# Kernel optimization log

Measured on AMD Instinct MI355X. Metric: run time of the kernel, lower is better.

Reference implementation:

```python
import jax, jax.numpy as jnp
import numpy as np

N, E, D_IN, HEADS, C = 100000, 1600000, 128, 4, 32  # C = out_channels per head


def setup_inputs() -> dict:
    key = jax.random.key(0)
    ks = jax.random.split(key, 10)
    s = 1.0 / np.sqrt(D_IN)
    return {
        "x": jax.random.normal(ks[0], (N, D_IN), jnp.float32),
        "edge_index": jax.random.randint(ks[1], (2, E), 0, N, jnp.int64),
        "Wq": jax.random.normal(ks[2], (D_IN, HEADS * C), jnp.float32) * s,
        "bq": jnp.zeros((HEADS * C,), jnp.float32),
        "Wk": jax.random.normal(ks[3], (D_IN, HEADS * C), jnp.float32) * s,
        "bk": jnp.zeros((HEADS * C,), jnp.float32),
        "Wv": jax.random.normal(ks[4], (D_IN, HEADS * C), jnp.float32) * s,
        "bv": jnp.zeros((HEADS * C,), jnp.float32),
        "Wskip": jax.random.normal(ks[5], (D_IN, HEADS * C), jnp.float32) * s,
        "bskip": jnp.zeros((HEADS * C,), jnp.float32),
    }


def reference(x, edge_index, Wq, bq, Wk, bk, Wv, bv, Wskip, bskip):
    n = x.shape[0]
    src, dst = edge_index[0], edge_index[1]  # message flows src (j) -> dst (i)
    q = (x @ Wq + bq).reshape(n, HEADS, C)
    k = (x @ Wk + bk).reshape(n, HEADS, C)
    v = (x @ Wv + bv).reshape(n, HEADS, C)

    # per-edge attention logits [E, H]
    alpha = jnp.einsum('ehc,ehc->eh', q[dst], k[src]) / jnp.sqrt(jnp.float32(C))

    # segment softmax over incoming edges of each target node
    m = jax.ops.segment_max(alpha, dst, num_segments=n)          # [N, H]
    p = jnp.exp(alpha - m[dst])                                   # [E, H]
    z = jax.ops.segment_sum(p, dst, num_segments=n)               # [N, H]
    w = p / (z[dst] + 1e-16)                                      # [E, H]

    # softmax-weighted scatter aggregation of values
    out = jax.ops.segment_sum(v[src] * w[:, :, None], dst, num_segments=n)
    out = out.reshape(n, HEADS * C)

    # root/skip connection (beta=False default: plain add)
    out = out + x @ Wskip + bskip
    return out
```

## Files before the change

### kernel.cpp

```cpp
#include <hip/hip_runtime.h>

#define DIN 128
#define NHEADS 4
#define CH 32
#define MT 128
#define CHUNK 4096
#define NPB 256
#define EPB_IT 25

typedef _Float16 h8 __attribute__((ext_vector_type(8)));
typedef float f4 __attribute__((ext_vector_type(4)));

__global__ __launch_bounds__(256) void cvt_x(
    const float* __restrict__ x, _Float16* __restrict__ xh, int n4)
{
    int i = blockIdx.x * 256 + threadIdx.x;
    if (i >= n4) return;
    float4 xv = reinterpret_cast<const float4*>(x)[i];
    _Float16 h[4] = {(_Float16)xv.x, (_Float16)xv.y, (_Float16)xv.z, (_Float16)xv.w};
    reinterpret_cast<uint2*>(xh)[i] = *reinterpret_cast<uint2*>(h);
}

__global__ __launch_bounds__(256) void prep_w(
    const float* __restrict__ Wq, const float* __restrict__ Wk,
    const float* __restrict__ Wv, const float* __restrict__ Wsk,
    _Float16* __restrict__ wt)
{
    int i = blockIdx.x * 256 + threadIdx.x;
    if (i >= 4 * 16384) return;
    int mat = i >> 14;
    int rem = i & 16383;
    int n  = rem >> 7;
    int kk = rem & 127;
    const float* W = (mat == 0) ? Wq : (mat == 1) ? Wk : (mat == 2) ? Wv : Wsk;
    wt[i] = (_Float16)W[kk * 128 + n];
}

__global__ __launch_bounds__(256) void qkvs_mfma(
    const _Float16* __restrict__ xh, const _Float16* __restrict__ wt,
    const float* __restrict__ bq, const float* __restrict__ bk,
    const float* __restrict__ bv, const float* __restrict__ bsk,
    _Float16* __restrict__ qh, _Float16* __restrict__ kvh,
    float* __restrict__ outskip, int N)
{
    __shared__ _Float16 As[MT * 128];
    const int t = threadIdx.x;
    const int rowBase = blockIdx.x * MT;
    const int mat = blockIdx.y;

    for (int i = t; i < MT * 16; i += 256) {
        int r  = i >> 4;
        int c8 = i & 15;
        uint4 val = make_uint4(0u, 0u, 0u, 0u);
        int gr = rowBase + r;
        if (gr < N)
            val = reinterpret_cast<const uint4*>(xh)[(size_t)gr * 16 + c8];
        *reinterpret_cast<uint4*>(&As[r * 128 + ((c8 ^ (r & 7)) << 3)]) = val;
    }
    __syncthreads();

    const int wid  = t >> 6;
    const int l    = t & 63;
    const int lm   = l & 15;
    const int quad = l >> 4;

    const _Float16* __restrict__ Bsrc = wt + (size_t)mat * 16384;

    f4 acc[2][8];
    #pragma unroll
    for (int ms = 0; ms < 2; ++ms)
        #pragma unroll
        for (int nt = 0; nt < 8; ++nt)
            acc[ms][nt] = (f4){0.f, 0.f, 0.f, 0.f};

    #pragma unroll
    for (int kq = 0; kq < 4; ++kq) {
        const int c8 = kq * 4 + quad;
        const int k0 = c8 << 3;
        h8 a0 = *reinterpret_cast<const h8*>(
            &As[(wid * 32 + lm) * 128 + ((c8 ^ (lm & 7)) << 3)]);
        h8 a1 = *reinterpret_cast<const h8*>(
            &As[(wid * 32 + 16 + lm) * 128 + ((c8 ^ (lm & 7)) << 3)]);
        #pragma unroll
        for (int nt = 0; nt < 8; ++nt) {
            h8 b = *reinterpret_cast<const h8*>(
                &Bsrc[(size_t)(nt * 16 + lm) * 128 + k0]);
            acc[0][nt] = __builtin_amdgcn_mfma_f32_16x16x32_f16(a0, b, acc[0][nt], 0, 0, 0);
            acc[1][nt] = __builtin_amdgcn_mfma_f32_16x16x32_f16(a1, b, acc[1][nt], 0, 0, 0);
        }
    }

    const float* bias = (mat == 0) ? bq : (mat == 1) ? bk : (mat == 2) ? bv : bsk;

    #pragma unroll
    for (int ms = 0; ms < 2; ++ms) {
        #pragma unroll
        for (int nt = 0; nt < 8; ++nt) {
            int col = nt * 16 + lm;
            float bsv = bias[col];
            #pragma unroll
            for (int i2 = 0; i2 < 4; ++i2) {
                int row = rowBase + wid * 32 + ms * 16 + quad * 4 + i2;
                if (row < N) {
                    float val = acc[ms][nt][i2] + bsv;
                    if (mat == 3)
                        outskip[(size_t)row * 128 + col] = val;
                    else if (mat == 0)
                        qh[(size_t)row * 128 + col] = (_Float16)val;
                    else {
                        size_t off = (size_t)row * 256 + ((col >> 2) << 3)
                                   + (col & 3) + ((mat == 2) ? 4 : 0);
                        kvh[off] = (_Float16)val;
                    }
                }
            }
        }
    }
}

__global__ __launch_bounds__(256) void bucket_hist(
    const int* __restrict__ ei, int* __restrict__ bcnt, int E, int nb)
{
    __shared__ int lds[512];
    for (int b = threadIdx.x; b < nb; b += 256) lds[b] = 0;
    __syncthreads();
    for (long long i = (long long)blockIdx.x * 256 + threadIdx.x; i < E;
         i += (long long)gridDim.x * 256)
        atomicAdd(&lds[ei[(size_t)E + i] >> 8], 1);
    __syncthreads();
    for (int b = threadIdx.x; b < nb; b += 256)
        if (lds[b]) atomicAdd(&bcnt[b], lds[b]);
}

__global__ __launch_bounds__(512) void scan_buckets(
    const int* __restrict__ bcnt, int* __restrict__ boff,
    int* __restrict__ bcur, int nb)
{
    __shared__ int ws[8];
    int t = threadIdx.x, lane = t & 63, wid = t >> 6;
    int v = (t < nb) ? bcnt[t] : 0;
    int s = v;
    #pragma unroll
    for (int off = 1; off < 64; off <<= 1) {
        int n = __shfl_up(s, off);
        if (lane >= off) s += n;
    }
    if (lane == 63) ws[wid] = s;
    __syncthreads();
    int add = 0;
    for (int w = 0; w < wid; ++w) add += ws[w];
    int excl = s - v + add;
    if (t < nb) { boff[t] = excl; bcur[t] = excl; }
    if (t == nb - 1) boff[nb] = excl + v;
}

__global__ __launch_bounds__(256) void bucket_scatter(
    const int* __restrict__ ei, int* __restrict__ bcur,
    uint2* __restrict__ pairs, int E, int nb)
{
    __shared__ int cnt[512];
    int t = threadIdx.x;
    for (int b = t; b < nb; b += 256) cnt[b] = 0;
    __syncthreads();

    long long e0 = (long long)blockIdx.x * (256 * EPB_IT);
    int ps[EPB_IT], pd[EPB_IT];
    #pragma unroll
    for (int j = 0; j < EPB_IT; ++j) {
        long long e = e0 + j * 256 + t;
        if (e < E) {
            ps[j] = ei[e];
            pd[j] = ei[(size_t)E + e];
            atomicAdd(&cnt[pd[j] >> 8], 1);
        } else pd[j] = -1;
    }
    __syncthreads();
    for (int b = t; b < nb; b += 256) {
        int c = cnt[b];
        if (c) cnt[b] = atomicAdd(&bcur[b], c);
    }
    __syncthreads();
    #pragma unroll
    for (int j = 0; j < EPB_IT; ++j) {
        if (pd[j] >= 0) {
            int pos = atomicAdd(&cnt[pd[j] >> 8], 1);
            pairs[pos] = make_uint2((unsigned)ps[j], (unsigned)pd[j]);
        }
    }
}

__global__ __launch_bounds__(256) void bucket_counts(
    const uint2* __restrict__ pairs, const int* __restrict__ boff,
    int* __restrict__ counts, int N)
{
    __shared__ int cnt[NPB];
    int b = blockIdx.x, t = threadIdx.x;
    cnt[t] = 0;
    __syncthreads();
    int s = boff[b], e = boff[b + 1];
    for (int i = s + t; i < e; i += 256)
        atomicAdd(&cnt[pairs[i].y & (NPB - 1)], 1);
    __syncthreads();
    int node = b * NPB + t;
    if (node < N) counts[node] = cnt[t];
}

__global__ __launch_bounds__(256) void chunk_sums(
    const int* __restrict__ counts, int* __restrict__ partials, int N)
{
    int b = blockIdx.x, t = threadIdx.x;
    int base = b * CHUNK + t * 16;
    int s = 0;
    #pragma unroll
    for (int j = 0; j < 16; ++j) {
        int i = base + j;
        if (i < N) s += counts[i];
    }
    #pragma unroll
    for (int off = 1; off < 64; off <<= 1) s += __shfl_xor(s, off);
    __shared__ int ws[4];
    int lane = t & 63, wid = t >> 6;
    if (lane == 0) ws[wid] = s;
    __syncthreads();
    if (t == 0) partials[b] = ws[0] + ws[1] + ws[2] + ws[3];
}

__global__ __launch_bounds__(256) void scan_chunks(
    const int* __restrict__ partials, int* __restrict__ chunkoff, int nch)
{
    __shared__ int ws[4];
    int t = threadIdx.x, lane = t & 63, wid = t >> 6;
    int v = (t < nch) ? partials[t] : 0;
    int s = v;
    #pragma unroll
    for (int off = 1; off < 64; off <<= 1) {
        int n = __shfl_up(s, off);
        if (lane >= off) s += n;
    }
    if (lane == 63) ws[wid] = s;
    __syncthreads();
    int add = 0;
    for (int w = 0; w < wid; ++w) add += ws[w];
    if (t < nch) chunkoff[t] = s - v + add;
}

__global__ __launch_bounds__(256) void scan_write(
    const int* __restrict__ counts, const int* __restrict__ chunkoff,
    int* __restrict__ rowptr, int N)
{
    int b = blockIdx.x, t = threadIdx.x;
    int base = b * CHUNK + t * 16;
    int vals[16];
    int s = 0;
    #pragma unroll
    for (int j = 0; j < 16; ++j) {
        int i = base + j;
        vals[j] = (i < N) ? counts[i] : 0;
        s += vals[j];
    }
    int lane = t & 63, wid = t >> 6;
    int incl = s;
    #pragma unroll
    for (int off = 1; off < 64; off <<= 1) {
        int n = __shfl_up(incl, off);
        if (lane >= off) incl += n;
    }
    __shared__ int ws[4];
    if (lane == 63) ws[wid] = incl;
    __syncthreads();
    int add = chunkoff[b];
    for (int w = 0; w < wid; ++w) add += ws[w];
    int run = incl - s + add;
    #pragma unroll
    for (int j = 0; j < 16; ++j) {
        int i = base + j;
        if (i < N) rowptr[i + 1] = run + vals[j];
        run += vals[j];
    }
    if (b == 0 && t == 0) rowptr[0] = 0;
}

__global__ __launch_bounds__(256) void bucket_place(
    const uint2* __restrict__ pairs, const int* __restrict__ boff,
    const int* __restrict__ rowptr, int* __restrict__ sorted, int N)
{
    __shared__ int cur[NPB];
    int b = blockIdx.x, t = threadIdx.x;
    int node = b * NPB + t;
    cur[t] = (node < N) ? rowptr[node] : 0;
    __syncthreads();
    int s = boff[b], e = boff[b + 1];
    for (int i = s + t; i < e; i += 256) {
        uint2 pr = pairs[i];
        int pos = atomicAdd(&cur[pr.y & (NPB - 1)], 1);
        sorted[pos] = (int)pr.x;
    }
}

__device__ inline float4 cvt4(uint2 r) {
    union { uint2 u; _Float16 h[4]; } c;
    c.u = r;
    return make_float4((float)c.h[0], (float)c.h[1], (float)c.h[2], (float)c.h[3]);
}

__global__ __launch_bounds__(256) void node_aggregate(
    const _Float16* __restrict__ q, const _Float16* __restrict__ kv,
    const int* __restrict__ rowptr, const int* __restrict__ srcs,
    float* __restrict__ out, int N)
{
    int gid  = blockIdx.x * 256 + threadIdx.x;
    int node = gid >> 5;
    if (node >= N) return;
    int l = gid & 31;

    float4 qv = cvt4(reinterpret_cast<const uint2*>(q + (size_t)node * 128)[l]);
    float4 acc = make_float4(0.f, 0.f, 0.f, 0.f);
    float z = 0.f;

    const uint4* kv4 = reinterpret_cast<const uint4*>(kv);
    const float SC = 0.17677669529663687f;
    int e0 = rowptr[node], e1 = rowptr[node + 1];
    int e = e0;
    for (; e + 4 <= e1; e += 4) {
        int s0 = srcs[e], s1 = srcs[e + 1], s2 = srcs[e + 2], s3 = srcs[e + 3];
        uint4 r0 = kv4[(size_t)s0 * 32 + l];
        uint4 r1 = kv4[(size_t)s1 * 32 + l];
        uint4 r2 = kv4[(size_t)s2 * 32 + l];
        uint4 r3 = kv4[(size_t)s3 * 32 + l];
        float4 k0 = cvt4(make_uint2(r0.x, r0.y)), v0 = cvt4(make_uint2(r0.z, r0.w));
        float4 k1 = cvt4(make_uint2(r1.x, r1.y)), v1 = cvt4(make_uint2(r1.z, r1.w));
        float4 k2 = cvt4(make_uint2(r2.x, r2.y)), v2 = cvt4(make_uint2(r2.z, r2.w));
        float4 k3 = cvt4(make_uint2(r3.x, r3.y)), v3 = cvt4(make_uint2(r3.z, r3.w));
        float sa = qv.x * k0.x + qv.y * k0.y + qv.z * k0.z + qv.w * k0.w;
        float sb = qv.x * k1.x + qv.y * k1.y + qv.z * k1.z + qv.w * k1.w;
        float sc = qv.x * k2.x + qv.y * k2.y + qv.z * k2.z + qv.w * k2.w;
        float sd = qv.x * k3.x + qv.y * k3.y + qv.z * k3.z + qv.w * k3.w;
        sa += __shfl_xor(sa, 1); sb += __shfl_xor(sb, 1);
        sc += __shfl_xor(sc, 1); sd += __shfl_xor(sd, 1);
        sa += __shfl_xor(sa, 2); sb += __shfl_xor(sb, 2);
        sc += __shfl_xor(sc, 2); sd += __shfl_xor(sd, 2);
        sa += __shfl_xor(sa, 4); sb += __shfl_xor(sb, 4);
        sc += __shfl_xor(sc, 4); sd += __shfl_xor(sd, 4);
        float pa = __expf(sa * SC), pb = __expf(sb * SC);
        float pc = __expf(sc * SC), pdd = __expf(sd * SC);
        z += (pa + pb) + (pc + pdd);
        acc.x += pa * v0.x + pb * v1.x + pc * v2.x + pdd * v3.x;
        acc.y += pa * v0.y + pb * v1.y + pc * v2.y + pdd * v3.y;
        acc.z += pa * v0.z + pb * v1.z + pc * v2.z + pdd * v3.z;
        acc.w += pa * v0.w + pb * v1.w + pc * v2.w + pdd * v3.w;
    }
    for (; e < e1; ++e) {
        int s0 = srcs[e];
        uint4 r0 = kv4[(size_t)s0 * 32 + l];
        float4 k0 = cvt4(make_uint2(r0.x, r0.y)), v0 = cvt4(make_uint2(r0.z, r0.w));
        float sa = qv.x * k0.x + qv.y * k0.y + qv.z * k0.z + qv.w * k0.w;
        sa += __shfl_xor(sa, 1);
        sa += __shfl_xor(sa, 2);
        sa += __shfl_xor(sa, 4);
        float pa = __expf(sa * SC);
        z += pa;
        acc.x += pa * v0.x; acc.y += pa * v0.y;
        acc.z += pa * v0.z; acc.w += pa * v0.w;
    }

    float inv = 1.f / (z + 1e-16f);
    float4 o = reinterpret_cast<float4*>(out)[(size_t)node * 32 + l];
    o.x += acc.x * inv; o.y += acc.y * inv;
    o.z += acc.z * inv; o.w += acc.w * inv;
    reinterpret_cast<float4*>(out)[(size_t)node * 32 + l] = o;
}

extern "C" void kernel_launch(void* const* d_in, const int* in_sizes, int n_in,
                              void* d_out, int out_size, void* d_ws, size_t ws_size,
                              hipStream_t stream)
{
    const float* x   = (const float*)d_in[0];
    const int*   ei  = (const int*)d_in[1];
    const float* Wq  = (const float*)d_in[2];
    const float* bq  = (const float*)d_in[3];
    const float* Wk  = (const float*)d_in[4];
    const float* bk  = (const float*)d_in[5];
    const float* Wv  = (const float*)d_in[6];
    const float* bv  = (const float*)d_in[7];
    const float* Wsk = (const float*)d_in[8];
    const float* bsk = (const float*)d_in[9];
    float* out = (float*)d_out;

    const int N = in_sizes[0] / DIN;
    const int E = in_sizes[1] / 2;
    const int nb = (N + NPB - 1) / NPB;

    _Float16* xh  = (_Float16*)d_ws;
    _Float16* qh  = xh + (size_t)N * DIN;
    _Float16* kvh = qh + (size_t)N * DIN;
    _Float16* wt  = kvh + (size_t)N * 256;
    uint2* pairs  = (uint2*)(wt + 4 * 16384);
    int* sorted   = (int*)(pairs + (size_t)E);
    int* counts   = sorted + E;
    int* rowptr   = counts + N;
    int* bcnt     = rowptr + (N + 1);
    int* boff     = bcnt + 512;
    int* bcur     = boff + 513;
    int* partials = bcur + 512;
    int* chunkoff = partials + 256;

    hipMemsetAsync(bcnt, 0, 512 * sizeof(int), stream);

    int n4 = N * DIN / 4;
    cvt_x<<<(n4 + 255) / 256, 256, 0, stream>>>(x, xh, n4);
    prep_w<<<(4 * 16384 + 255) / 256, 256, 0, stream>>>(Wq, Wk, Wv, Wsk, wt);

    dim3 ggrid((N + MT - 1) / MT, 4);
    qkvs_mfma<<<ggrid, 256, 0, stream>>>(xh, wt, bq, bk, bv, bsk,
                                         qh, kvh, out, N);

    bucket_hist<<<256, 256, 0, stream>>>(ei, bcnt, E, nb);
    scan_buckets<<<1, 512, 0, stream>>>(bcnt, boff, bcur, nb);
    int sb = (E + 256 * EPB_IT - 1) / (256 * EPB_IT);
    bucket_scatter<<<sb, 256, 0, stream>>>(ei, bcur, pairs, E, nb);
    bucket_counts<<<nb, 256, 0, stream>>>(pairs, boff, counts, N);

    int nch = (N + CHUNK - 1) / CHUNK;
    chunk_sums<<<nch, 256, 0, stream>>>(counts, partials, N);
    scan_chunks<<<1, 256, 0, stream>>>(partials, chunkoff, nch);
    scan_write<<<nch, 256, 0, stream>>>(counts, chunkoff, rowptr, N);

    bucket_place<<<nb, 256, 0, stream>>>(pairs, boff, rowptr, sorted, N);

    int ab = (N * 32 + 255) / 256;
    node_aggregate<<<ab, 256, 0, stream>>>(qh, kvh, rowptr, sorted, out, N);
}
```

Measured before the change: 438.2 us.

## Fuse x fp16 conversion into projection GEMM and compute all four matrices per block

Drops the separate cvt_x kernel and converts fp32 x to fp16 while loading it into shared memory inside the GEMM kernel. Each block now loads its x tile once, keeps the A fragments in registers, and loops over the Q, K, V and skip weight matrices instead of launching four grid slices that each reload x. Outputs are staged through padded shared memory so q, kv and skip results go to global memory as vectorized, coalesced stores rather than scattered scalar writes. This trades a smaller grid with more serial work and extra barriers per block for less global traffic and one fewer launch.

```diff
diff --git a/kernel.cpp b/kernel.cpp
--- a/kernel.cpp
+++ b/kernel.cpp
@@ -8,18 +8,11 @@
 #define NPB 256
 #define EPB_IT 25
 
+#define ST_H 136
+#define ST_F 132
+
 typedef _Float16 h8 __attribute__((ext_vector_type(8)));
 typedef float f4 __attribute__((ext_vector_type(4)));
-
-__global__ __launch_bounds__(256) void cvt_x(
-    const float* __restrict__ x, _Float16* __restrict__ xh, int n4)
-{
-    int i = blockIdx.x * 256 + threadIdx.x;
-    if (i >= n4) return;
-    float4 xv = reinterpret_cast<const float4*>(x)[i];
-    _Float16 h[4] = {(_Float16)xv.x, (_Float16)xv.y, (_Float16)xv.z, (_Float16)xv.w};
-    reinterpret_cast<uint2*>(xh)[i] = *reinterpret_cast<uint2*>(h);
-}
 
 __global__ __launch_bounds__(256) void prep_w(
     const float* __restrict__ Wq, const float* __restrict__ Wk,
@@ -36,26 +29,35 @@
     wt[i] = (_Float16)W[kk * 128 + n];
 }
 
-__global__ __launch_bounds__(256) void qkvs_mfma(
-    const _Float16* __restrict__ xh, const _Float16* __restrict__ wt,
+__global__ __launch_bounds__(256) void qkvs_all(
+    const float* __restrict__ x, const _Float16* __restrict__ wt,
     const float* __restrict__ bq, const float* __restrict__ bk,
     const float* __restrict__ bv, const float* __restrict__ bsk,
     _Float16* __restrict__ qh, _Float16* __restrict__ kvh,
     float* __restrict__ outskip, int N)
 {
-    __shared__ _Float16 As[MT * 128];
+    __shared__ _Float16 Sbuf[17408];
     const int t = threadIdx.x;
     const int rowBase = blockIdx.x * MT;
-    const int mat = blockIdx.y;
 
     for (int i = t; i < MT * 16; i += 256) {
         int r  = i >> 4;
         int c8 = i & 15;
-        uint4 val = make_uint4(0u, 0u, 0u, 0u);
         int gr = rowBase + r;
-        if (gr < N)
-            val = reinterpret_cast<const uint4*>(xh)[(size_t)gr * 16 + c8];
-        *reinterpret_cast<uint4*>(&As[r * 128 + ((c8 ^ (r & 7)) << 3)]) = val;
+        _Float16 h[8];
+        if (gr < N) {
+            float4 f0 = reinterpret_cast<const float4*>(x)[(size_t)gr * 32 + c8 * 2];
+            float4 f1 = reinterpret_cast<const float4*>(x)[(size_t)gr * 32 + c8 * 2 + 1];
+            h[0] = (_Float16)f0.x; h[1] = (_Float16)f0.y;
+            h[2] = (_Float16)f0.z; h[3] = (_Float16)f0.w;
+            h[4] = (_Float16)f1.x; h[5] = (_Float16)f1.y;
+            h[6] = (_Float16)f1.z; h[7] = (_Float16)f1.w;
+        } else {
+            #pragma unroll
+            for (int j = 0; j < 8; ++j) h[j] = (_Float16)0.f;
+        }
+        *reinterpret_cast<uint4*>(&Sbuf[r * 128 + ((c8 ^ (r & 7)) << 3)]) =
+            *reinterpret_cast<uint4*>(h);
     }
     __syncthreads();
 
@@ -64,55 +66,105 @@
     const int lm   = l & 15;
     const int quad = l >> 4;
 
-    const _Float16* __restrict__ Bsrc = wt + (size_t)mat * 16384;
-
-    f4 acc[2][8];
-    #pragma unroll
-    for (int ms = 0; ms < 2; ++ms)
+    h8 afrag[2][4];
+    #pragma unroll
+    for (int kq = 0; kq < 4; ++kq) {
+        int c8 = kq * 4 + quad;
+        afrag[0][kq] = *reinterpret_cast<const h8*>(
+            &Sbuf[(wid * 32 + lm) * 128 + ((c8 ^ (lm & 7)) << 3)]);
+        afrag[1][kq] = *reinterpret_cast<const h8*>(
+            &Sbuf[(wid * 32 + 16 + lm) * 128 + ((c8 ^ (lm & 7)) << 3)]);
+    }
+    __syncthreads();
+
+    for (int mat = 0; mat < 4; ++mat) {
+        const _Float16* __restrict__ Bsrc = wt + (size_t)mat * 16384;
+
+        f4 acc[2][8];
         #pragma unroll
-        for (int nt = 0; nt < 8; ++nt)
-            acc[ms][nt] = (f4){0.f, 0.f, 0.f, 0.f};
-
-    #pragma unroll
-    for (int kq = 0; kq < 4; ++kq) {
-        const int c8 = kq * 4 + quad;
-        const int k0 = c8 << 3;
-        h8 a0 = *reinterpret_cast<const h8*>(
-            &As[(wid * 32 + lm) * 128 + ((c8 ^ (lm & 7)) << 3)]);
-        h8 a1 = *reinterpret_cast<const h8*>(
-            &As[(wid * 32 + 16 + lm) * 128 + ((c8 ^ (lm & 7)) << 3)]);
+        for (int ms = 0; ms < 2; ++ms)
+            #pragma unroll
+            for (int nt = 0; nt < 8; ++nt)
+                acc[ms][nt] = (f4){0.f, 0.f, 0.f, 0.f};
+
         #pragma unroll
-        for (int nt = 0; nt < 8; ++nt) {
-            h8 b = *reinterpret_cast<const h8*>(
-                &Bsrc[(size_t)(nt * 16 + lm) * 128 + k0]);
-            acc[0][nt] = __builtin_amdgcn_mfma_f32_16x16x32_f16(a0, b, acc[0][nt], 0, 0, 0);
-            acc[1][nt] = __builtin_amdgcn_mfma_f32_16x16x32_f16(a1, b, acc[1][nt], 0, 0, 0);
+        for (int kq = 0; kq < 4; ++kq) {
+            const int k0 = (kq * 4 + quad) << 3;
+            #pragma unroll
+            for (int nt = 0; nt < 8; ++nt) {
+                h8 b = *reinterpret_cast<const h8*>(
+                    &Bsrc[(size_t)(nt * 16 + lm) * 128 + k0]);
+                acc[0][nt] = __builtin_amdgcn_mfma_f32_16x16x32_f16(afrag[0][kq], b, acc[0][nt], 0, 0, 0);
+                acc[1][nt] = __builtin_amdgcn_mfma_f32_16x16x32_f16(afrag[1][kq], b, acc[1][nt], 0, 0, 0);
+            }
         }
-    }
-
-    const float* bias = (mat == 0) ? bq : (mat == 1) ? bk : (mat == 2) ? bv : bsk;
-
-    #pragma unroll
-    for (int ms = 0; ms < 2; ++ms) {
-        #pragma unroll
-        for (int nt = 0; nt < 8; ++nt) {
-            int col = nt * 16 + lm;
-            float bsv = bias[col];
+
+        const float* bias = (mat == 0) ? bq : (mat == 1) ? bk : (mat == 2) ? bv : bsk;
+
+        if (mat < 3) {
             #pragma unroll
-            for (int i2 = 0; i2 < 4; ++i2) {
-                int row = rowBase + wid * 32 + ms * 16 + quad * 4 + i2;
-                if (row < N) {
-                    float val = acc[ms][nt][i2] + bsv;
-                    if (mat == 3)
-                        outskip[(size_t)row * 128 + col] = val;
-                    else if (mat == 0)
-                        qh[(size_t)row * 128 + col] = (_Float16)val;
-                    else {
-                        size_t off = (size_t)row * 256 + ((col >> 2) << 3)
-                                   + (col & 3) + ((mat == 2) ? 4 : 0);
-                        kvh[off] = (_Float16)val;
+            for (int ms = 0; ms < 2; ++ms) {
+                #pragma unroll
+                for (int nt = 0; nt < 8; ++nt) {
+                    int col = nt * 16 + lm;
+                    float bsv = bias[col];
+                    int row = wid * 32 + ms * 16 + quad * 4;
+                    #pragma unroll
+                    for (int i2 = 0; i2 < 4; ++i2)
+                        Sbuf[(row + i2) * ST_H + col] = (_Float16)(acc[ms][nt][i2] + bsv);
+                }
+            }
+            __syncthreads();
+            if (mat == 0) {
+                for (int j = t; j < 2048; j += 256) {
+                    int r  = j >> 4;
+                    int c0 = (j & 15) << 3;
+                    int gr = rowBase + r;
+                    if (gr < N)
+                        *reinterpret_cast<uint4*>(&qh[(size_t)gr * 128 + c0]) =
+                            *reinterpret_cast<const uint4*>(&Sbuf[r * ST_H + c0]);
+                }
+            } else {
+                const int koff = (mat == 2) ? 4 : 0;
+                for (int j = t; j < 4096; j += 256) {
+                    int r = j >> 5;
+                    int g = j & 31;
+                    int gr = rowBase + r;
+                    if (gr < N)
+                        *reinterpret_cast<uint2*>(&kvh[(size_t)gr * 256 + g * 8 + koff]) =
+                            *reinterpret_cast<const uint2*>(&Sbuf[r * ST_H + g * 4]);
+                }
+            }
+            __syncthreads();
+        } else {
+            float* Sf = reinterpret_cast<float*>(Sbuf);
+            #pragma unroll
+            for (int p = 0; p < 2; ++p) {
+                if ((wid >> 1) == p) {
+                    int lrow = (wid & 1) * 32;
+                    #pragma unroll
+                    for (int ms = 0; ms < 2; ++ms) {
+                        #pragma unroll
+                        for (int nt = 0; nt < 8; ++nt) {
+                            int col = nt * 16 + lm;
+                            float bsv = bias[col];
+                            int row = lrow + ms * 16 + quad * 4;
+                            #pragma unroll
+                            for (int i2 = 0; i2 < 4; ++i2)
+                                Sf[(row + i2) * ST_F + col] = acc[ms][nt][i2] + bsv;
+                        }
                     }
                 }
+                __syncthreads();
+                for (int j = t; j < 2048; j += 256) {
+                    int r  = j >> 5;
+                    int c0 = (j & 31) << 2;
+                    int gr = rowBase + p * 64 + r;
+                    if (gr < N)
+                        *reinterpret_cast<float4*>(&outskip[(size_t)gr * 128 + c0]) =
+                            *reinterpret_cast<const float4*>(&Sf[r * ST_F + c0]);
+                }
+                __syncthreads();
             }
         }
     }
@@ -390,8 +442,7 @@
     const int E = in_sizes[1] / 2;
     const int nb = (N + NPB - 1) / NPB;
 
-    _Float16* xh  = (_Float16*)d_ws;
-    _Float16* qh  = xh + (size_t)N * DIN;
+    _Float16* qh  = (_Float16*)d_ws;
     _Float16* kvh = qh + (size_t)N * DIN;
     _Float16* wt  = kvh + (size_t)N * 256;
     uint2* pairs  = (uint2*)(wt + 4 * 16384);
@@ -406,13 +457,10 @@
 
     hipMemsetAsync(bcnt, 0, 512 * sizeof(int), stream);
 
-    int n4 = N * DIN / 4;
-    cvt_x<<<(n4 + 255) / 256, 256, 0, stream>>>(x, xh, n4);
     prep_w<<<(4 * 16384 + 255) / 256, 256, 0, stream>>>(Wq, Wk, Wv, Wsk, wt);
 
-    dim3 ggrid((N + MT - 1) / MT, 4);
-    qkvs_mfma<<<ggrid, 256, 0, stream>>>(xh, wt, bq, bk, bv, bsk,
-                                         qh, kvh, out, N);
+    qkvs_all<<<(N + MT - 1) / MT, 256, 0, stream>>>(x, wt, bq, bk, bv, bsk,
+                                                    qh, kvh, out, N);
 
     bucket_hist<<<256, 256, 0, stream>>>(ei, bcnt, E, nb);
     scan_buckets<<<1, 512, 0, stream>>>(bcnt, boff, bcur, nb);
```

Result: faster. 398.8 us (-9.0%).
